# Performance work log

Hardware: AMD Instinct MI355X
Metric: run time of the kernel (lower is better)

The kernel has to match this reference:

```python
import jax, jax.numpy as jnp
import numpy as np
import math
from jax import lax

B, C, T = 32, 256, 1024
KS = 64          # key_size
KERN = 3         # conv kernel size
PAD = 2          # (KERN-1)*dilation, chomped -> causal left pad
SQRT_KS = math.sqrt(KS)


def setup_inputs() -> dict:
    key = jax.random.key(0)
    ks = jax.random.split(key, 14)
    s = 0.01
    return {
        "x":  jax.random.normal(ks[0], (B, C, T), jnp.float32),
        # attention linears (stored [in, out])
        "wq": jax.random.normal(ks[1], (C, KS), jnp.float32) * s,
        "bq": jnp.zeros((KS,), jnp.float32),
        "wk": jax.random.normal(ks[2], (C, KS), jnp.float32) * s,
        "bk": jnp.zeros((KS,), jnp.float32),
        "wv": jax.random.normal(ks[3], (C, C), jnp.float32) * s,
        "bv": jnp.zeros((C,), jnp.float32),
        # weight-normed conv 1: v [out,in,k], g [out], b [out]
        "v1": jax.random.normal(ks[4], (C, C, KERN), jnp.float32) * s,
        "g1": jnp.ones((C,), jnp.float32),
        "b1": jnp.zeros((C,), jnp.float32),
        # weight-normed conv 2
        "v2": jax.random.normal(ks[5], (C, C, KERN), jnp.float32) * s,
        "g2": jnp.ones((C,), jnp.float32),
        "b2": jnp.zeros((C,), jnp.float32),
    }


def _wn_conv_relu(h, v, g, b):
    # weight_norm (dim=0): W = g * v / ||v||, norm over (in, k) per out channel
    norm = jnp.sqrt(jnp.sum(v * v, axis=(1, 2), keepdims=True))
    W = (g[:, None, None] / norm) * v
    # left-pad PAD == Conv1d(padding=PAD) + Chomp1d(PAD)  (causal conv)
    y = lax.conv_general_dilated(h, W, window_strides=(1,), padding=[(PAD, 0)],
                                 dimension_numbers=("NCH", "OIH", "NCH"))
    return jax.nn.relu(y + b[None, :, None])


def reference(x, wq, bq, wk, bk, wv, bv, v1, g1, b1, v2, g2, b2):
    t = x.shape[2]
    xt = jnp.swapaxes(x, 1, 2)                      # [B, T, C]
    q = xt @ wq + bq                                # [B, T, KS]
    k = xt @ wk + bk                                # [B, T, KS]
    v = xt @ wv + bv                                # [B, T, C]
    scores = jnp.einsum("bqd,bkd->bqk", q, k)       # [B, Tq, Tk]
    # torch mask[j][i] = 1 if i > j -> masked where key index > query index
    idx = jnp.arange(t)
    mask = idx[None, :] > idx[:, None]              # [Tq, Tk]
    scores = jnp.where(mask[None], -jnp.inf, scores)
    # NOTE: source applies softmax over dim=1 (the QUERY axis) — faithful quirk
    attn = jax.nn.softmax(scores / SQRT_KS, axis=1)  # [B, Tq, Tk]
    out_attn = jnp.einsum("bqk,bkc->bqc", attn, v)  # [B, T, C]
    out_attn = jnp.swapaxes(out_attn, 1, 2)         # [B, C, T]
    # conv stack (dropout=0 / eval)
    out = _wn_conv_relu(out_attn, v1, g1, b1)
    out = _wn_conv_relu(out, v2, g2, b2)
    # en_res branch: per-timestep scaling of x by softmaxed attention mass
    weight_x = jax.nn.softmax(jnp.sum(attn, axis=2), axis=1)  # [B, T]
    en_res_x = weight_x[:, None, :] * x                       # [B, C, T]
    # downsample is None (n_inputs == n_outputs)
    return jax.nn.relu(out + x + en_res_x)
```

## Files before the change

kernel.cpp:

```cpp
#include <hip/hip_runtime.h>
#include <math.h>

#define BB 32
#define CC 256
#define TT 1024

typedef __attribute__((ext_vector_type(4))) float f4;
typedef __attribute__((ext_vector_type(4))) float f32x4;
typedef __attribute__((ext_vector_type(16))) float f32x16;
typedef __attribute__((ext_vector_type(8))) short s8;
typedef __attribute__((ext_vector_type(4))) short s4v;

__device__ inline short f2bf(float f) {
    unsigned u = __builtin_bit_cast(unsigned, f);
    u = (u + 0x7FFFu + ((u >> 16) & 1u)) >> 16;
    return (short)u;
}

static const size_t OFF_QBF  = 0;
static const size_t OFF_KBF  = 4194304;
static const size_t OFF_VT   = 8388608;
static const size_t OFF_OA   = 25165824;
static const size_t OFF_C1   = 58720256;
static const size_t OFF_CRZ  = 75497472;
static const size_t OFF_RS   = 75628544;
static const size_t OFF_WX   = 75759616;
static const size_t OFF_W1   = 75890688;
static const size_t OFF_W2   = 76283904;
static const size_t OFF_WQKV = 76677120;

__global__ __launch_bounds__(256)
void wn_kernel(const float* __restrict__ v1, const float* __restrict__ g1,
               const float* __restrict__ v2, const float* __restrict__ g2,
               short* __restrict__ w1bf, short* __restrict__ w2bf) {
    __shared__ float red[4];
    int which = blockIdx.x >> 8, o = blockIdx.x & 255;
    const float* v = which ? v2 : v1;
    const float* g = which ? g2 : g1;
    short* wt = which ? w2bf : w1bf;
    const float* row = v + (size_t)o * 768;
    int tid = threadIdx.x, lane = tid & 63, wv_ = tid >> 6;
    float r0 = row[tid], r1 = row[tid + 256], r2 = row[tid + 512];
    float s = r0 * r0 + r1 * r1 + r2 * r2;
    for (int d = 1; d < 64; d <<= 1) s += __shfl_xor(s, d, 64);
    if (lane == 0) red[wv_] = s;
    __syncthreads();
    float scale = g[o] * rsqrtf(red[0] + red[1] + red[2] + red[3]);
    for (int j = 0; j < 3; ++j)
        wt[((size_t)(j * 256 + o)) * 256 + tid] = f2bf(scale * row[tid * 3 + j]);
}

__global__ __launch_bounds__(256)
void pack_kernel(const float* __restrict__ wq, const float* __restrict__ wk,
                 const float* __restrict__ wv, short* __restrict__ wqkvbf) {
    int n = blockIdx.x * 4 + (threadIdx.x >> 6);
    int c0 = (threadIdx.x & 63) * 4;
    for (int p = 0; p < 4; ++p) {
        int c = c0 + p;
        float w;
        if (n < 64)       w = wq[c * 64 + n];
        else if (n < 128) w = wk[c * 64 + n - 64];
        else              w = wv[c * 256 + n - 128];
        wqkvbf[(size_t)n * 256 + c] = f2bf(w);
    }
}

__global__ void transpose_kernel(const float* __restrict__ x, short* __restrict__ xt) {
    __shared__ float Tt[64 * 68];
    int tid = threadIdx.x;
    int c0 = blockIdx.x * 64, t0 = blockIdx.y * 64, b = blockIdx.z;
    for (int it = 0; it < 4; ++it) {
        int idx = tid + 256 * it;
        int cr = idx >> 4, tc = idx & 15;
        f4 v = *reinterpret_cast<const f4*>(&x[((size_t)b * CC + c0 + cr) * TT + t0 + tc * 4]);
        *reinterpret_cast<f4*>(&Tt[cr * 68 + tc * 4]) = v;
    }
    __syncthreads();
    for (int it = 0; it < 2; ++it) {
        int idx = tid + 256 * it;
        int tl = idx >> 3, seg = idx & 7;
        s8 o;
        for (int p = 0; p < 8; ++p) o[p] = f2bf(Tt[(seg * 8 + p) * 68 + tl]);
        *reinterpret_cast<s8*>(&xt[((size_t)b * TT + t0 + tl) * CC + c0 + seg * 8]) = o;
    }
}

__global__ __launch_bounds__(256, 3)
void qkv_kernel(const short* __restrict__ xt, const short* __restrict__ wqkv,
                const float* __restrict__ bq, const float* __restrict__ bk,
                const float* __restrict__ bv,
                short* __restrict__ qbf, short* __restrict__ kbf, short* __restrict__ vt) {
    __shared__ short SL[128 * 72 + 64 * 72];
    short* Asm = SL;
    short* Bsm = SL + 128 * 72;
    int tid = threadIdx.x, wv_ = tid >> 6, lane = tid & 63;
    int n15 = lane & 15, quad = lane >> 4;
    int bid = blockIdx.x;
    int r = bid & 7, n = (bid >> 3) % 6, qd = bid / 48;
    int bt = qd * 8 + r;
    int b = bt >> 3, t0 = (bt & 7) * 128;
    int n0 = n * 64;

    f32x4 acc[2][4];
    for (int i = 0; i < 2; ++i) for (int j = 0; j < 4; ++j)
        for (int p = 0; p < 4; ++p) acc[i][j][p] = 0.f;

    for (int kc = 0; kc < 4; ++kc) {
        int c0 = kc * 64;
        __syncthreads();
        for (int it = 0; it < 4; ++it) {
            int idx = tid + 256 * it;
            int row = idx >> 3, seg = idx & 7;
            *reinterpret_cast<s8*>(&Asm[row * 72 + seg * 8]) =
                *reinterpret_cast<const s8*>(&xt[((size_t)b * TT + t0 + row) * CC + c0 + seg * 8]);
        }
        for (int it = 0; it < 2; ++it) {
            int idx = tid + 256 * it;
            int row = idx >> 3, seg = idx & 7;
            *reinterpret_cast<s8*>(&Bsm[row * 72 + seg * 8]) =
                *reinterpret_cast<const s8*>(&wqkv[(size_t)(n0 + row) * 256 + c0 + seg * 8]);
        }
        __syncthreads();
        for (int ks = 0; ks < 2; ++ks)
            for (int mt2 = 0; mt2 < 2; ++mt2) {
                s8 a = *reinterpret_cast<const s8*>(&Asm[(wv_ * 32 + mt2 * 16 + n15) * 72 + quad * 8 + ks * 32]);
                for (int nt = 0; nt < 4; ++nt) {
                    s8 bb = *reinterpret_cast<const s8*>(&Bsm[(nt * 16 + n15) * 72 + quad * 8 + ks * 32]);
                    acc[mt2][nt] = __builtin_amdgcn_mfma_f32_16x16x32_bf16(a, bb, acc[mt2][nt], 0, 0, 0);
                }
            }
    }
    if (n0 < 128) {
        short* outp = (n0 == 0) ? qbf : kbf;
        const float* bias = (n0 == 0) ? bq : bk;
        for (int mt2 = 0; mt2 < 2; ++mt2)
            for (int nt = 0; nt < 4; ++nt) {
                int n_ = nt * 16 + n15;
                float bvl = bias[n_];
                for (int reg = 0; reg < 4; ++reg) {
                    int t = t0 + wv_ * 32 + mt2 * 16 + quad * 4 + reg;
                    outp[((size_t)b * TT + t) * 64 + n_] = f2bf(acc[mt2][nt][reg] + bvl);
                }
            }
    } else {
        int cbase = n0 - 128;
        __syncthreads();
        short* Tw = SL + wv_ * 3072;
        for (int mt2 = 0; mt2 < 2; ++mt2)
            for (int nt = 0; nt < 4; ++nt) {
                int n_ = nt * 16 + n15;
                float bvl = bv[cbase + n_];
                for (int reg = 0; reg < 4; ++reg)
                    Tw[n_ * 48 + mt2 * 16 + quad * 4 + reg] = f2bf(acc[mt2][nt][reg] + bvl);
            }
        for (int p = 0; p < 4; ++p) {
            int n_ = (lane >> 2) + 16 * p;
            int seg = lane & 3;
            s8 vv = *reinterpret_cast<const s8*>(&Tw[n_ * 48 + seg * 8]);
            *reinterpret_cast<s8*>(&vt[((size_t)b * CC + cbase + n_) * TT + t0 + wv_ * 32 + seg * 8]) = vv;
        }
    }
}

__global__ __launch_bounds__(512, 2)
void colz_kernel(const short* __restrict__ qbf, const short* __restrict__ kbf,
                 float* __restrict__ colrz) {
    __shared__ short Qs[4][64 * 72];
    __shared__ short Ks[64 * 72];
    __shared__ float redz[8][2][32];
    int tid = threadIdx.x, wv_ = tid >> 6, lane = tid & 63;
    int l31 = lane & 31, lh = lane >> 5;
    int qh = wv_ & 1, ti = wv_ >> 1;
    int b = blockIdx.x & 31, pr = blockIdx.x >> 5;
    int kts[2] = {pr, 15 - pr};
    int row = tid >> 3, sg = (tid & 7) * 8;

    s8 kr = *reinterpret_cast<const s8*>(&kbf[((size_t)b * TT + kts[0] * 64 + row) * 64 + sg]);
    s8 qreg[4];
    for (int j = 0; j < 4; ++j) {
        int t = kts[0] + j; if (t > 15) t = 15;
        qreg[j] = *reinterpret_cast<const s8*>(&qbf[((size_t)b * TT + t * 64 + row) * 64 + sg]);
    }

    for (int ph = 0; ph < 2; ++ph) {
        int kt = kts[ph];
        float zl[2] = {0.f, 0.f};
        for (int u = kt; u < 16; u += 4) {
            __syncthreads();
            if (u == kt) *reinterpret_cast<s8*>(&Ks[row * 72 + sg]) = kr;
            for (int j = 0; j < 4; ++j)
                *reinterpret_cast<s8*>(&Qs[j][row * 72 + sg]) = qreg[j];
            __syncthreads();
            int nu = u + 4;
            if (nu < 16) {
                for (int j = 0; j < 4; ++j) {
                    int t = nu + j; if (t > 15) t = 15;
                    qreg[j] = *reinterpret_cast<const s8*>(&qbf[((size_t)b * TT + t * 64 + row) * 64 + sg]);
                }
            } else if (ph == 0) {
                int k2 = kts[1];
                kr = *reinterpret_cast<const s8*>(&kbf[((size_t)b * TT + k2 * 64 + row) * 64 + sg]);
                for (int j = 0; j < 4; ++j) {
                    int t = k2 + j; if (t > 15) t = 15;
                    qreg[j] = *reinterpret_cast<const s8*>(&qbf[((size_t)b * TT + t * 64 + row) * 64 + sg]);
                }
            }
            int qtw = u + ti;
            if (qtw < 16) {
                for (int kh = 0; kh < 2; ++kh) {
                    f32x16 s;
                    for (int p = 0; p < 16; ++p) s[p] = 0.f;
                    for (int kc = 0; kc < 4; ++kc) {
                        s8 a  = *reinterpret_cast<const s8*>(&Qs[ti][(qh * 32 + l31) * 72 + kc * 16 + lh * 8]);
                        s8 bb = *reinterpret_cast<const s8*>(&Ks[(kh * 32 + l31) * 72 + kc * 16 + lh * 8]);
                        s = __builtin_amdgcn_mfma_f32_32x32x16_bf16(a, bb, s, 0, 0, 0);
                    }
                    int kg = kt * 64 + kh * 32 + l31;
                    int qb0 = qtw * 64 + qh * 32 + 4 * lh;
                    if (qtw > kt) {
                        for (int reg = 0; reg < 16; ++reg)
                            zl[kh] += __expf(s[reg] * 0.125f);
                    } else {
                        for (int reg = 0; reg < 16; ++reg) {
                            int rr = (reg & 3) + 8 * (reg >> 2);
                            if (qb0 + rr >= kg) zl[kh] += __expf(s[reg] * 0.125f);
                        }
                    }
                }
            }
        }
        for (int kh = 0; kh < 2; ++kh) {
            float zc = zl[kh] + __shfl_xor(zl[kh], 32, 64);
            if (lane < 32) redz[wv_][kh][lane] = zc;
        }
        __syncthreads();
        if (tid < 64) {
            int kh = tid >> 5, kk = tid & 31;
            float Z = 0.f;
            for (int w = 0; w < 8; ++w) Z += redz[w][kh][kk];
            colrz[(size_t)b * TT + kt * 64 + tid] = 1.0f / Z;
        }
        __syncthreads();
    }
}

__global__ __launch_bounds__(512, 4)
void attn_kernel(const short* __restrict__ qbf, const short* __restrict__ kbf,
                 const short* __restrict__ vt, const float* __restrict__ colrz,
                 short* __restrict__ oab, float* __restrict__ rowsum) {
    __shared__ short Qs[32 * 72];
    __shared__ short Ks[64 * 72];
    __shared__ short Ps[32 * 72];
    __shared__ short Vs[256 * 72];
    __shared__ float redR[2][32];
    int tid = threadIdx.x, wv_ = tid >> 6, lane = tid & 63;
    int l31 = lane & 31, lh = lane >> 5;
    int wk2 = wv_ & 1, wdup = wv_ >> 1;
    int bid = blockIdx.x;
    int b = bid & 31, pr = (bid >> 5) & 7, qh = bid >> 8;
    int qts[2] = {15 - pr, pr};
    int row = tid >> 3, sg = (tid & 7) * 8;

    s8 kreg, vreg[4];
    {
        kreg = *reinterpret_cast<const s8*>(&kbf[((size_t)b * TT + row) * 64 + sg]);
        for (int it = 0; it < 4; ++it) {
            int idx = tid + 512 * it;
            int vr = idx >> 3, seg = idx & 7;
            vreg[it] = *reinterpret_cast<const s8*>(&vt[((size_t)b * CC + vr) * TT + seg * 8]);
        }
    }

    for (int ph = 0; ph < 2; ++ph) {
        int qt = qts[ph];
        s8 qr0;
        if (tid < 256)
            qr0 = *reinterpret_cast<const s8*>(
                &qbf[((size_t)b * TT + qt * 64 + qh * 32 + row) * 64 + sg]);
        f32x16 acc;
        for (int p = 0; p < 16; ++p) acc[p] = 0.f;
        float rsum[4] = {0.f, 0.f, 0.f, 0.f};

        for (int kt = 0; kt <= qt; ++kt) {
            __syncthreads();
            if (kt == 0 && tid < 256) *reinterpret_cast<s8*>(&Qs[row * 72 + sg]) = qr0;
            *reinterpret_cast<s8*>(&Ks[row * 72 + sg]) = kreg;
            for (int it = 0; it < 4; ++it) {
                int idx = tid + 512 * it;
                int vr = idx >> 3, seg = idx & 7;
                *reinterpret_cast<s8*>(&Vs[vr * 72 + seg * 8]) = vreg[it];
            }
            __syncthreads();
            int nkt = (kt < qt) ? kt + 1 : ((ph == 0) ? 0 : -1);
            if (nkt >= 0) {
                kreg = *reinterpret_cast<const s8*>(&kbf[((size_t)b * TT + nkt * 64 + row) * 64 + sg]);
                for (int it = 0; it < 4; ++it) {
                    int idx = tid + 512 * it;
                    int vr = idx >> 3, seg = idx & 7;
                    vreg[it] = *reinterpret_cast<const s8*>(&vt[((size_t)b * CC + vr) * TT + nkt * 64 + seg * 8]);
                }
            }
            f32x16 s;
            for (int p = 0; p < 16; ++p) s[p] = 0.f;
            for (int kc = 0; kc < 4; ++kc) {
                s8 a  = *reinterpret_cast<const s8*>(&Qs[l31 * 72 + kc * 16 + lh * 8]);
                s8 bb = *reinterpret_cast<const s8*>(&Ks[(wk2 * 32 + l31) * 72 + kc * 16 + lh * 8]);
                s = __builtin_amdgcn_mfma_f32_32x32x16_bf16(a, bb, s, 0, 0, 0);
            }
            int kg = kt * 64 + wk2 * 32 + l31;
            float rz = colrz[(size_t)b * TT + kg];
            bool full = (kt < qt);
            int qb0 = qt * 64 + qh * 32 + 4 * lh;
            for (int r = 0; r < 4; ++r) {
                int reg = wdup * 4 + r;
                int rr = (reg & 3) + 8 * (reg >> 2);
                float p = 0.f;
                if (full || qb0 + rr >= kg) p = __expf(s[reg] * 0.125f) * rz;
                rsum[r] += p;
                Ps[(rr + 4 * lh) * 72 + wk2 * 32 + l31] = f2bf(p);
            }
            __syncthreads();
            for (int kc = 0; kc < 4; ++kc) {
                s8 a  = *reinterpret_cast<const s8*>(&Ps[l31 * 72 + kc * 16 + lh * 8]);
                s8 bb = *reinterpret_cast<const s8*>(&Vs[(wv_ * 32 + l31) * 72 + kc * 16 + lh * 8]);
                acc = __builtin_amdgcn_mfma_f32_32x32x16_bf16(a, bb, acc, 0, 0, 0);
            }
        }
        for (int r = 0; r < 4; ++r) {
            float v = rsum[r];
            v += __shfl_xor(v, 1, 64);
            v += __shfl_xor(v, 2, 64);
            v += __shfl_xor(v, 4, 64);
            v += __shfl_xor(v, 8, 64);
            v += __shfl_xor(v, 16, 64);
            int reg = wdup * 4 + r;
            int rr = (reg & 3) + 8 * (reg >> 2);
            if (l31 == 0) redR[wk2][rr + 4 * lh] = v;
        }
        {
            int c = wv_ * 32 + l31;
            for (int reg = 0; reg < 16; ++reg) {
                int q = qt * 64 + qh * 32 + (reg & 3) + 8 * (reg >> 2) + 4 * lh;
                oab[((size_t)b * TT + q) * CC + c] = f2bf(acc[reg]);
            }
        }
        __syncthreads();
        if (tid < 32)
            rowsum[(size_t)b * TT + qt * 64 + qh * 32 + tid] = redR[0][tid] + redR[1][tid];
        __syncthreads();
    }
}

__global__ __launch_bounds__(256, 3)
void conv_kernel(const void* __restrict__ inp, int in_is_fp32,
                 const short* __restrict__ wbf, const float* __restrict__ bias,
                 void* __restrict__ outp, int out_is_bf16,
                 const float* __restrict__ xres, const float* __restrict__ wxv,
                 int fuse_final) {
    __shared__ short SL[130 * 72 + 3 * 64 * 72];
    short* As = SL;
    short* Bs = SL + 130 * 72;
    int tid = threadIdx.x, wv_ = tid >> 6, lane = tid & 63;
    int n15 = lane & 15, quad = lane >> 4;
    int bid = blockIdx.x;
    int r = bid & 7;
    int n0 = ((bid >> 3) & 3) << 6;
    int bm = (bid >> 5) * 8 + r;
    int b = bm >> 3, mt = bm & 7;
    int t0 = mt * 128;
    f32x4 acc[2][4];
    for (int i = 0; i < 2; ++i) for (int j = 0; j < 4; ++j)
        for (int p = 0; p < 4; ++p) acc[i][j][p] = 0.f;

    for (int kc = 0; kc < 4; ++kc) {
        int c0 = kc * 64;
        __syncthreads();
        if (in_is_fp32) {
            const float* in = (const float*)inp;
            for (int it = 0; it < 9; ++it) {
                int idx = tid + 256 * it;
                int row = idx >> 4, fc = idx & 15;
                if (row < 130) {
                    int t = t0 + row - 2;
                    s4v st;
                    if (t >= 0) {
                        f4 v = *reinterpret_cast<const f4*>(&in[((size_t)b * TT + t) * CC + c0 + fc * 4]);
                        for (int p = 0; p < 4; ++p) st[p] = f2bf(v[p]);
                    } else { for (int p = 0; p < 4; ++p) st[p] = 0; }
                    *reinterpret_cast<s4v*>(&As[row * 72 + fc * 4]) = st;
                }
            }
        } else {
            const short* in = (const short*)inp;
            for (int it = 0; it < 5; ++it) {
                int idx = tid + 256 * it;
                int row = idx >> 3, seg = idx & 7;
                if (row < 130) {
                    int t = t0 + row - 2;
                    s8 st;
                    if (t >= 0) st = *reinterpret_cast<const s8*>(&in[((size_t)b * TT + t) * CC + c0 + seg * 8]);
                    else for (int p = 0; p < 8; ++p) st[p] = 0;
                    *reinterpret_cast<s8*>(&As[row * 72 + seg * 8]) = st;
                }
            }
        }
        for (int it = 0; it < 6; ++it) {
            int idx = tid + 256 * it;
            int row = idx >> 3, seg = idx & 7;
            int j = row >> 6, o = row & 63;
            *reinterpret_cast<s8*>(&Bs[row * 72 + seg * 8]) =
                *reinterpret_cast<const s8*>(&wbf[((size_t)(j * 256 + n0 + o)) * 256 + c0 + seg * 8]);
        }
        __syncthreads();
        for (int j = 0; j < 3; ++j)
            for (int ks = 0; ks < 2; ++ks)
                for (int mt2 = 0; mt2 < 2; ++mt2) {
                    s8 a = *reinterpret_cast<const s8*>(&As[(wv_ * 32 + mt2 * 16 + n15 + j) * 72 + quad * 8 + ks * 32]);
                    for (int nt = 0; nt < 4; ++nt) {
                        s8 bb = *reinterpret_cast<const s8*>(&Bs[(j * 64 + nt * 16 + n15) * 72 + quad * 8 + ks * 32]);
                        acc[mt2][nt] = __builtin_amdgcn_mfma_f32_16x16x32_bf16(a, bb, acc[mt2][nt], 0, 0, 0);
                    }
                }
    }
    if (!fuse_final) {
        for (int mt2 = 0; mt2 < 2; ++mt2)
            for (int nt = 0; nt < 4; ++nt) {
                int o = n0 + nt * 16 + n15;
                float bvl = bias[o];
                for (int reg = 0; reg < 4; ++reg) {
                    int t = t0 + wv_ * 32 + mt2 * 16 + quad * 4 + reg;
                    float v = fmaxf(acc[mt2][nt][reg] + bvl, 0.f);
                    if (out_is_bf16) ((short*)outp)[((size_t)b * TT + t) * CC + o] = f2bf(v);
                    else             ((float*)outp)[((size_t)b * TT + t) * CC + o] = v;
                }
            }
    } else {
        float* Ft = (float*)SL;
        __syncthreads();
        for (int mt2 = 0; mt2 < 2; ++mt2)
            for (int nt = 0; nt < 4; ++nt) {
                int ol = nt * 16 + n15;
                float bvl = bias[n0 + ol];
                for (int reg = 0; reg < 4; ++reg) {
                    int tl = wv_ * 32 + mt2 * 16 + quad * 4 + reg;
                    Ft[tl * 67 + ol] = fmaxf(acc[mt2][nt][reg] + bvl, 0.f);
                }
            }
        __syncthreads();
        int c_l = tid >> 5;
        int t_l = (tid & 31) * 4;
        f4 wv4 = *reinterpret_cast<const f4*>(&wxv[(size_t)b * TT + t0 + t_l]);
        for (int pass = 0; pass < 8; ++pass) {
            int c = n0 + pass * 8 + c_l;
            f4 xv = *reinterpret_cast<const f4*>(&xres[((size_t)b * CC + c) * TT + t0 + t_l]);
            f4 rr;
            for (int p = 0; p < 4; ++p)
                rr[p] = fmaxf(Ft[(t_l + p) * 67 + pass * 8 + c_l] + xv[p] * (1.f + wv4[p]), 0.f);
            *reinterpret_cast<f4*>(&((float*)outp)[((size_t)b * CC + c) * TT + t0 + t_l]) = rr;
        }
    }
}

__global__ void rowsm_kernel(const float* __restrict__ rowsum, float* __restrict__ wx) {
    __shared__ float red[256];
    int b = blockIdx.x, tid = threadIdx.x;
    float v[4];
    float m = -1e30f;
    for (int r = 0; r < 4; ++r) { v[r] = rowsum[(size_t)b * TT + tid + 256 * r]; m = fmaxf(m, v[r]); }
    red[tid] = m; __syncthreads();
    for (int s = 128; s > 0; s >>= 1) { if (tid < s) red[tid] = fmaxf(red[tid], red[tid + s]); __syncthreads(); }
    m = red[0]; __syncthreads();
    float e[4], zs = 0.f;
    for (int r = 0; r < 4; ++r) { e[r] = __expf(v[r] - m); zs += e[r]; }
    red[tid] = zs; __syncthreads();
    for (int s = 128; s > 0; s >>= 1) { if (tid < s) red[tid] += red[tid + s]; __syncthreads(); }
    float rz = 1.0f / red[0];
    for (int r = 0; r < 4; ++r) wx[(size_t)b * TT + tid + 256 * r] = e[r] * rz;
}

extern "C" void kernel_launch(void* const* d_in, const int* in_sizes, int n_in,
                              void* d_out, int out_size, void* d_ws, size_t ws_size,
                              hipStream_t stream) {
    (void)in_sizes; (void)n_in; (void)out_size; (void)ws_size;
    const float* x  = (const float*)d_in[0];
    const float* wq = (const float*)d_in[1];
    const float* bq = (const float*)d_in[2];
    const float* wk = (const float*)d_in[3];
    const float* bk = (const float*)d_in[4];
    const float* wv = (const float*)d_in[5];
    const float* bv = (const float*)d_in[6];
    const float* v1 = (const float*)d_in[7];
    const float* g1 = (const float*)d_in[8];
    const float* b1 = (const float*)d_in[9];
    const float* v2 = (const float*)d_in[10];
    const float* g2 = (const float*)d_in[11];
    const float* b2 = (const float*)d_in[12];
    char* ws = (char*)d_ws;
    float* out = (float*)d_out;

    short* qbf  = (short*)(ws + OFF_QBF);
    short* kbf  = (short*)(ws + OFF_KBF);
    short* vt   = (short*)(ws + OFF_VT);
    short* xt   = (short*)(ws + OFF_OA);
    short* oab  = (short*)(ws + OFF_OA);
    short* c1   = (short*)(ws + OFF_C1);
    float* crz  = (float*)(ws + OFF_CRZ);
    float* rs   = (float*)(ws + OFF_RS);
    float* wxb  = (float*)(ws + OFF_WX);
    short* w1bf = (short*)(ws + OFF_W1);
    short* w2bf = (short*)(ws + OFF_W2);
    short* wqkv = (short*)(ws + OFF_WQKV);

    wn_kernel<<<dim3(512), dim3(256), 0, stream>>>(v1, g1, v2, g2, w1bf, w2bf);
    pack_kernel<<<dim3(96), dim3(256), 0, stream>>>(wq, wk, wv, wqkv);
    transpose_kernel<<<dim3(4, 16, 32), dim3(256), 0, stream>>>(x, xt);
    qkv_kernel<<<dim3(1536), dim3(256), 0, stream>>>(xt, wqkv, bq, bk, bv, qbf, kbf, vt);
    colz_kernel<<<dim3(256), dim3(512), 0, stream>>>(qbf, kbf, crz);
    attn_kernel<<<dim3(512), dim3(512), 0, stream>>>(qbf, kbf, vt, crz, oab, rs);
    rowsm_kernel<<<dim3(32), dim3(256), 0, stream>>>(rs, wxb);
    conv_kernel<<<dim3(1024), dim3(256), 0, stream>>>(oab, 0, w1bf, b1, c1, 1,
                                                      nullptr, nullptr, 0);
    conv_kernel<<<dim3(1024), dim3(256), 0, stream>>>(c1, 0, w2bf, b2, out, 0,
                                                      x, wxb, 1);
}
```

Before: 235.4 us.

## Store Q/K/V in MFMA fragment order and load attention operands directly from global

The QKV projection now writes Q, K and V^T in a pre-swizzled fragment layout that matches MFMA operand order, and colz reads through the new layout. The attention kernel drops its LDS staging of Q, K, V and P. Each wave loads fragments straight from global memory, computes S^T so probabilities can be repacked in registers with a cross-half shuffle, and splits key tiles by parity across wave pairs, reducing the partial outputs through LDS at the end. This removes most barriers and LDS traffic, but loses the cross-wave reuse of K/V tiles and raises global load volume and register pressure.

```diff
diff --git a/kernel.cpp b/kernel.cpp
--- a/kernel.cpp
+++ b/kernel.cpp
@@ -10,11 +10,17 @@
 typedef __attribute__((ext_vector_type(16))) float f32x16;
 typedef __attribute__((ext_vector_type(8))) short s8;
 typedef __attribute__((ext_vector_type(4))) short s4v;
+typedef __attribute__((ext_vector_type(4))) int i32x4;
 
 __device__ inline short f2bf(float f) {
     unsigned u = __builtin_bit_cast(unsigned, f);
     u = (u + 0x7FFFu + ((u >> 16) & 1u)) >> 16;
     return (short)u;
+}
+
+__device__ inline size_t fo_qk(int b, int t64, int row, int sg) {
+    int th = row >> 5, tl = row & 31, kc = sg >> 4, lhh = (sg >> 3) & 1;
+    return ((((((size_t)b * 16 + t64) * 2 + th) * 4 + kc) * 2 + lhh) * 32 + tl) * 8;
 }
 
 static const size_t OFF_QBF  = 0;
@@ -136,10 +142,13 @@
         for (int mt2 = 0; mt2 < 2; ++mt2)
             for (int nt = 0; nt < 4; ++nt) {
                 int n_ = nt * 16 + n15;
+                int kc = n_ >> 4, lhh = (n_ >> 3) & 1, j = n_ & 7;
                 float bvl = bias[n_];
                 for (int reg = 0; reg < 4; ++reg) {
                     int t = t0 + wv_ * 32 + mt2 * 16 + quad * 4 + reg;
-                    outp[((size_t)b * TT + t) * 64 + n_] = f2bf(acc[mt2][nt][reg] + bvl);
+                    int tt = t >> 6, th = (t >> 5) & 1, tl = t & 31;
+                    size_t idx = ((((((size_t)b * 16 + tt) * 2 + th) * 4 + kc) * 2 + lhh) * 32 + tl) * 8 + j;
+                    outp[idx] = f2bf(acc[mt2][nt][reg] + bvl);
                 }
             }
     } else {
@@ -157,7 +166,12 @@
             int n_ = (lane >> 2) + 16 * p;
             int seg = lane & 3;
             s8 vv = *reinterpret_cast<const s8*>(&Tw[n_ * 48 + seg * 8]);
-            *reinterpret_cast<s8*>(&vt[((size_t)b * CC + cbase + n_) * TT + t0 + wv_ * 32 + seg * 8]) = vv;
+            int c = cbase + n_;
+            int t = t0 + wv_ * 32 + seg * 8;
+            int kt = t >> 6, tl = t & 63;
+            int kc = tl >> 4, lhh = (tl >> 3) & 1;
+            size_t idx = ((((((size_t)b * 16 + kt) * 8 + (c >> 5)) * 4 + kc) * 2 + lhh) * 32 + (c & 31)) * 8;
+            *reinterpret_cast<s8*>(&vt[idx]) = vv;
         }
     }
 }
@@ -175,11 +189,11 @@
     int kts[2] = {pr, 15 - pr};
     int row = tid >> 3, sg = (tid & 7) * 8;
 
-    s8 kr = *reinterpret_cast<const s8*>(&kbf[((size_t)b * TT + kts[0] * 64 + row) * 64 + sg]);
+    s8 kr = *reinterpret_cast<const s8*>(&kbf[fo_qk(b, kts[0], row, sg)]);
     s8 qreg[4];
     for (int j = 0; j < 4; ++j) {
         int t = kts[0] + j; if (t > 15) t = 15;
-        qreg[j] = *reinterpret_cast<const s8*>(&qbf[((size_t)b * TT + t * 64 + row) * 64 + sg]);
+        qreg[j] = *reinterpret_cast<const s8*>(&qbf[fo_qk(b, t, row, sg)]);
     }
 
     for (int ph = 0; ph < 2; ++ph) {
@@ -195,14 +209,14 @@
             if (nu < 16) {
                 for (int j = 0; j < 4; ++j) {
                     int t = nu + j; if (t > 15) t = 15;
-                    qreg[j] = *reinterpret_cast<const s8*>(&qbf[((size_t)b * TT + t * 64 + row) * 64 + sg]);
+                    qreg[j] = *reinterpret_cast<const s8*>(&qbf[fo_qk(b, t, row, sg)]);
                 }
             } else if (ph == 0) {
                 int k2 = kts[1];
-                kr = *reinterpret_cast<const s8*>(&kbf[((size_t)b * TT + k2 * 64 + row) * 64 + sg]);
+                kr = *reinterpret_cast<const s8*>(&kbf[fo_qk(b, k2, row, sg)]);
                 for (int j = 0; j < 4; ++j) {
                     int t = k2 + j; if (t > 15) t = 15;
-                    qreg[j] = *reinterpret_cast<const s8*>(&qbf[((size_t)b * TT + t * 64 + row) * 64 + sg]);
+                    qreg[j] = *reinterpret_cast<const s8*>(&qbf[fo_qk(b, t, row, sg)]);
                 }
             }
             int qtw = u + ti;
@@ -244,110 +258,113 @@
     }
 }
 
-__global__ __launch_bounds__(512, 4)
+__global__ __launch_bounds__(256, 2)
 void attn_kernel(const short* __restrict__ qbf, const short* __restrict__ kbf,
                  const short* __restrict__ vt, const float* __restrict__ colrz,
                  short* __restrict__ oab, float* __restrict__ rowsum) {
-    __shared__ short Qs[32 * 72];
-    __shared__ short Ks[64 * 72];
-    __shared__ short Ps[32 * 72];
-    __shared__ short Vs[256 * 72];
-    __shared__ float redR[2][32];
+    __shared__ float Om[2][32 * 261];
+    __shared__ float redS[2][32];
     int tid = threadIdx.x, wv_ = tid >> 6, lane = tid & 63;
     int l31 = lane & 31, lh = lane >> 5;
-    int wk2 = wv_ & 1, wdup = wv_ >> 1;
-    int bid = blockIdx.x;
-    int b = bid & 31, pr = (bid >> 5) & 7, qh = bid >> 8;
-    int qts[2] = {15 - pr, pr};
-    int row = tid >> 3, sg = (tid & 7) * 8;
-
-    s8 kreg, vreg[4];
-    {
-        kreg = *reinterpret_cast<const s8*>(&kbf[((size_t)b * TT + row) * 64 + sg]);
-        for (int it = 0; it < 4; ++it) {
-            int idx = tid + 512 * it;
-            int vr = idx >> 3, seg = idx & 7;
-            vreg[it] = *reinterpret_cast<const s8*>(&vt[((size_t)b * CC + vr) * TT + seg * 8]);
-        }
-    }
+    int par = wv_ & 1, ch = wv_ >> 1;
+    int b = blockIdx.x & 31, pr = blockIdx.x >> 5;
+    int tiles[2] = {31 - pr, pr};
 
     for (int ph = 0; ph < 2; ++ph) {
-        int qt = qts[ph];
-        s8 qr0;
-        if (tid < 256)
-            qr0 = *reinterpret_cast<const s8*>(
-                &qbf[((size_t)b * TT + qt * 64 + qh * 32 + row) * 64 + sg]);
-        f32x16 acc;
-        for (int p = 0; p < 16; ++p) acc[p] = 0.f;
-        float rsum[4] = {0.f, 0.f, 0.f, 0.f};
-
-        for (int kt = 0; kt <= qt; ++kt) {
-            __syncthreads();
-            if (kt == 0 && tid < 256) *reinterpret_cast<s8*>(&Qs[row * 72 + sg]) = qr0;
-            *reinterpret_cast<s8*>(&Ks[row * 72 + sg]) = kreg;
-            for (int it = 0; it < 4; ++it) {
-                int idx = tid + 512 * it;
-                int vr = idx >> 3, seg = idx & 7;
-                *reinterpret_cast<s8*>(&Vs[vr * 72 + seg * 8]) = vreg[it];
-            }
-            __syncthreads();
-            int nkt = (kt < qt) ? kt + 1 : ((ph == 0) ? 0 : -1);
-            if (nkt >= 0) {
-                kreg = *reinterpret_cast<const s8*>(&kbf[((size_t)b * TT + nkt * 64 + row) * 64 + sg]);
-                for (int it = 0; it < 4; ++it) {
-                    int idx = tid + 512 * it;
-                    int vr = idx >> 3, seg = idx & 7;
-                    vreg[it] = *reinterpret_cast<const s8*>(&vt[((size_t)b * CC + vr) * TT + nkt * 64 + seg * 8]);
-                }
-            }
+        int qi = tiles[ph];
+        int qt64 = qi >> 1, qh = qi & 1;
+        s8 qf[4];
+        #pragma unroll
+        for (int kc = 0; kc < 4; ++kc)
+            qf[kc] = *reinterpret_cast<const s8*>(
+                &qbf[((((((size_t)b * 16 + qt64) * 2 + qh) * 4 + kc) * 2 + lh) * 32 + l31) * 8]);
+        f32x16 acc[4];
+        #pragma unroll
+        for (int i = 0; i < 4; ++i)
+            for (int p = 0; p < 16; ++p) acc[i][p] = 0.f;
+        float rsum = 0.f;
+        int qg = qi * 32 + l31;
+
+        for (int kt = par; kt <= qi; kt += 2) {
+            int kt64 = kt >> 1, kh = kt & 1;
+            s8 kf[4];
+            #pragma unroll
+            for (int kc = 0; kc < 4; ++kc)
+                kf[kc] = *reinterpret_cast<const s8*>(
+                    &kbf[((((((size_t)b * 16 + kt64) * 2 + kh) * 4 + kc) * 2 + lh) * 32 + l31) * 8]);
+            s8 vf[8];
+            #pragma unroll
+            for (int ctl = 0; ctl < 4; ++ctl)
+                for (int h = 0; h < 2; ++h) {
+                    int kc = kh * 2 + h;
+                    vf[ctl * 2 + h] = *reinterpret_cast<const s8*>(
+                        &vt[((((((size_t)b * 16 + kt64) * 8 + (ch * 4 + ctl)) * 4 + kc) * 2 + lh) * 32 + l31) * 8]);
+                }
             f32x16 s;
+            #pragma unroll
             for (int p = 0; p < 16; ++p) s[p] = 0.f;
-            for (int kc = 0; kc < 4; ++kc) {
-                s8 a  = *reinterpret_cast<const s8*>(&Qs[l31 * 72 + kc * 16 + lh * 8]);
-                s8 bb = *reinterpret_cast<const s8*>(&Ks[(wk2 * 32 + l31) * 72 + kc * 16 + lh * 8]);
-                s = __builtin_amdgcn_mfma_f32_32x32x16_bf16(a, bb, s, 0, 0, 0);
-            }
-            int kg = kt * 64 + wk2 * 32 + l31;
-            float rz = colrz[(size_t)b * TT + kg];
-            bool full = (kt < qt);
-            int qb0 = qt * 64 + qh * 32 + 4 * lh;
-            for (int r = 0; r < 4; ++r) {
-                int reg = wdup * 4 + r;
-                int rr = (reg & 3) + 8 * (reg >> 2);
-                float p = 0.f;
-                if (full || qb0 + rr >= kg) p = __expf(s[reg] * 0.125f) * rz;
-                rsum[r] += p;
-                Ps[(rr + 4 * lh) * 72 + wk2 * 32 + l31] = f2bf(p);
-            }
-            __syncthreads();
-            for (int kc = 0; kc < 4; ++kc) {
-                s8 a  = *reinterpret_cast<const s8*>(&Ps[l31 * 72 + kc * 16 + lh * 8]);
-                s8 bb = *reinterpret_cast<const s8*>(&Vs[(wv_ * 32 + l31) * 72 + kc * 16 + lh * 8]);
-                acc = __builtin_amdgcn_mfma_f32_32x32x16_bf16(a, bb, acc, 0, 0, 0);
-            }
-        }
-        for (int r = 0; r < 4; ++r) {
-            float v = rsum[r];
-            v += __shfl_xor(v, 1, 64);
-            v += __shfl_xor(v, 2, 64);
-            v += __shfl_xor(v, 4, 64);
-            v += __shfl_xor(v, 8, 64);
-            v += __shfl_xor(v, 16, 64);
-            int reg = wdup * 4 + r;
-            int rr = (reg & 3) + 8 * (reg >> 2);
-            if (l31 == 0) redR[wk2][rr + 4 * lh] = v;
-        }
-        {
-            int c = wv_ * 32 + l31;
-            for (int reg = 0; reg < 16; ++reg) {
-                int q = qt * 64 + qh * 32 + (reg & 3) + 8 * (reg >> 2) + 4 * lh;
-                oab[((size_t)b * TT + q) * CC + c] = f2bf(acc[reg]);
-            }
-        }
-        __syncthreads();
+            #pragma unroll
+            for (int kc = 0; kc < 4; ++kc)
+                s = __builtin_amdgcn_mfma_f32_32x32x16_bf16(kf[kc], qf[kc], s, 0, 0, 0);
+            float p[16];
+            int kb0 = kt * 32;
+            #pragma unroll
+            for (int r = 0; r < 16; ++r) {
+                int kg = kb0 + (r & 3) + 8 * (r >> 2) + 4 * lh;
+                float rz = colrz[(size_t)b * TT + kg];
+                float pv = 0.f;
+                if (kg <= qg) pv = __expf(s[r] * 0.125f) * rz;
+                p[r] = pv;
+                rsum += pv;
+            }
+            unsigned w[8], x[8];
+            #pragma unroll
+            for (int r2 = 0; r2 < 8; ++r2) {
+                unsigned lo = (unsigned short)f2bf(p[2 * r2]);
+                unsigned hi = (unsigned short)f2bf(p[2 * r2 + 1]);
+                w[r2] = lo | (hi << 16);
+            }
+            #pragma unroll
+            for (int i = 0; i < 8; ++i)
+                x[i] = (unsigned)__shfl_xor((int)w[i], 32, 64);
+            #pragma unroll
+            for (int h = 0; h < 2; ++h) {
+                i32x4 fi;
+                if (lh == 0) {
+                    fi[0] = (int)w[4 * h];     fi[1] = (int)w[4 * h + 1];
+                    fi[2] = (int)x[4 * h];     fi[3] = (int)x[4 * h + 1];
+                } else {
+                    fi[0] = (int)x[4 * h + 2]; fi[1] = (int)x[4 * h + 3];
+                    fi[2] = (int)w[4 * h + 2]; fi[3] = (int)w[4 * h + 3];
+                }
+                s8 pb = __builtin_bit_cast(s8, fi);
+                #pragma unroll
+                for (int ctl = 0; ctl < 4; ++ctl)
+                    acc[ctl] = __builtin_amdgcn_mfma_f32_32x32x16_bf16(vf[ctl * 2 + h], pb, acc[ctl], 0, 0, 0);
+            }
+        }
+        __syncthreads();
+        #pragma unroll
+        for (int ctl = 0; ctl < 4; ++ctl)
+            for (int r = 0; r < 16; ++r) {
+                int c = ch * 128 + ctl * 32 + (r & 3) + 8 * (r >> 2) + 4 * lh;
+                Om[par][l31 * 261 + c] = acc[ctl][r];
+            }
+        float rtot = rsum + __shfl_xor(rsum, 32, 64);
+        if (ch == 0 && lane < 32) redS[par][lane] = rtot;
+        __syncthreads();
+        for (int u = tid; u < 1024; u += 256) {
+            int row = u >> 5, seg = u & 31;
+            s8 o;
+            #pragma unroll
+            for (int j = 0; j < 8; ++j) {
+                float v = Om[0][row * 261 + seg * 8 + j] + Om[1][row * 261 + seg * 8 + j];
+                o[j] = f2bf(v);
+            }
+            *reinterpret_cast<s8*>(&oab[((size_t)b * TT + qi * 32 + row) * CC + seg * 8]) = o;
+        }
         if (tid < 32)
-            rowsum[(size_t)b * TT + qt * 64 + qh * 32 + tid] = redR[0][tid] + redR[1][tid];
-        __syncthreads();
+            rowsum[(size_t)b * TT + qi * 32 + tid] = redS[0][tid] + redS[1][tid];
     }
 }
 
@@ -516,7 +533,7 @@
     transpose_kernel<<<dim3(4, 16, 32), dim3(256), 0, stream>>>(x, xt);
     qkv_kernel<<<dim3(1536), dim3(256), 0, stream>>>(xt, wqkv, bq, bk, bv, qbf, kbf, vt);
     colz_kernel<<<dim3(256), dim3(512), 0, stream>>>(qbf, kbf, crz);
-    attn_kernel<<<dim3(512), dim3(512), 0, stream>>>(qbf, kbf, vt, crz, oab, rs);
+    attn_kernel<<<dim3(512), dim3(256), 0, stream>>>(qbf, kbf, vt, crz, oab, rs);
     rowsm_kernel<<<dim3(32), dim3(256), 0, stream>>>(rs, wxb);
     conv_kernel<<<dim3(1024), dim3(256), 0, stream>>>(oab, 0, w1bf, b1, c1, 1,
                                                       nullptr, nullptr, 0);
```

New measurement: 247.3 us. +5.0%, slower.
